# Kernel optimization log

Hardware: AMD Instinct MI355X
Metric: run time of the kernel (lower is better)

Reference implementation:

```python
import jax, jax.numpy as jnp
import numpy as np

NC, NG, NP = 8192, 4096, 140
FD, D, L = 512, 256, 2
E_OBS, E_COEXP, E_PPI, E_SYM = 300000, 200000, 10000, 20000
EPS = 1e-5


def layer_norm(x, g, b):
    mu = jnp.mean(x, -1, keepdims=True)
    v = jnp.mean((x - mu) ** 2, -1, keepdims=True)
    return (x - mu) * jax.lax.rsqrt(v + EPS) * g + b


def sage(h_src, h_dst, src, dst, w, Ws, Wn, b, n_dst):
    # DGL SAGEConv (mean aggregator, edge-weighted): mean over incoming
    # weighted messages, then fc_self(h_dst) + fc_neigh(neigh) + bias.
    m = h_src[src] * w[:, None]                                  # [E, D]
    neigh = jax.ops.segment_sum(m, dst, num_segments=n_dst)      # [n_dst, D]
    deg = jax.ops.segment_sum(jnp.ones_like(w), dst, num_segments=n_dst)
    neigh = neigh / jnp.maximum(deg, 1.0)[:, None]
    return h_dst @ Ws + neigh @ Wn + b


def setup_inputs() -> dict:
    key = jax.random.key(0)
    ks = iter(jax.random.split(key, 64))
    def n(*s):
        return jax.random.normal(next(ks), s, jnp.float32) * 0.02
    def u(e):
        return jax.random.uniform(next(ks), (e,), jnp.float32)
    def ri(e, hi):
        return jax.random.randint(next(ks), (e,), 0, hi, jnp.int32)
    return dict(
        cell_feat=jax.random.normal(next(ks), (NC, FD), jnp.float32),
        gene_feat=jax.random.normal(next(ks), (NG, FD), jnp.float32),
        pro_idx=jnp.arange(NP, dtype=jnp.int32),
        obs_src=ri(E_OBS, NG), obs_dst=ri(E_OBS, NC), obs_w=u(E_OBS),
        rev_obs_src=ri(E_OBS, NC), rev_obs_dst=ri(E_OBS, NG), rev_obs_w=u(E_OBS),
        symbol_src=ri(E_SYM, NG), symbol_dst=ri(E_SYM, NP), symbol_w=u(E_SYM),
        rev_symbol_src=ri(E_SYM, NP), rev_symbol_dst=ri(E_SYM, NG), rev_symbol_w=u(E_SYM),
        coexp_src=ri(E_COEXP, NG), coexp_dst=ri(E_COEXP, NG), coexp_w=u(E_COEXP),
        ppi_src=ri(E_PPI, NP), ppi_dst=ri(E_PPI, NP), ppi_w=u(E_PPI),
        W_emb_cell=n(FD, D), b_emb_cell=jnp.zeros((D,), jnp.float32),
        W_emb_gene=n(FD, D), b_emb_gene=jnp.zeros((D,), jnp.float32),
        emb_pro=n(NP, D),
        W_mlpcell=n(L, D, D), b_mlpcell=jnp.zeros((L, D), jnp.float32),
        W_sage_self=n(L, 6, D, D), W_sage_neigh=n(L, 6, D, D),
        b_sage=jnp.zeros((L, 6, D), jnp.float32),
        ln1_g=jnp.ones((L, 3, D), jnp.float32), ln1_b=jnp.zeros((L, 3, D), jnp.float32),
        ln2_g=jnp.ones((L, 3, D), jnp.float32), ln2_b=jnp.zeros((L, 3, D), jnp.float32),
        W_last=n(3 * D, NP), b_last=jnp.zeros((NP,), jnp.float32),
    )


def reference(cell_feat, gene_feat, pro_idx,
              obs_src, obs_dst, obs_w,
              rev_obs_src, rev_obs_dst, rev_obs_w,
              symbol_src, symbol_dst, symbol_w,
              rev_symbol_src, rev_symbol_dst, rev_symbol_w,
              coexp_src, coexp_dst, coexp_w,
              ppi_src, ppi_dst, ppi_w,
              W_emb_cell, b_emb_cell, W_emb_gene, b_emb_gene, emb_pro,
              W_mlpcell, b_mlpcell, W_sage_self, W_sage_neigh, b_sage,
              ln1_g, ln1_b, ln2_g, ln2_b, W_last, b_last):
    act = jax.nn.selu
    hc = cell_feat @ W_emb_cell + b_emb_cell      # emb_cell
    hg = gene_feat @ W_emb_gene + b_emb_gene      # emb_gene
    hp = emb_pro[pro_idx]                         # nn.Embedding path
    nc, ng, npn = hc.shape[0], hg.shape[0], hp.shape[0]
    hist = [hc]
    for l in range(W_mlpcell.shape[0]):
        Ws, Wn, bs = W_sage_self[l], W_sage_neigh[l], b_sage[l]
        hmlp = layer_norm(act(hc @ W_mlpcell[l] + b_mlpcell[l]), ln1_g[l, 2], ln1_b[l, 2])
        # HeteroGraphConv(SAGE) over edges_sub = [obs, rev_obs, symbol, rev_symbol] (stack)
        s_obs = sage(hg, hc, obs_src, obs_dst, obs_w, Ws[0], Wn[0], bs[0], nc)
        s_robs = sage(hc, hg, rev_obs_src, rev_obs_dst, rev_obs_w, Ws[1], Wn[1], bs[1], ng)
        s_sym = sage(hg, hp, symbol_src, symbol_dst, symbol_w, Ws[2], Wn[2], bs[2], npn)
        s_rsym = sage(hp, hg, rev_symbol_src, rev_symbol_dst, rev_symbol_w, Ws[3], Wn[3], bs[3], ng)
        # homogeneous subgraph convs: gene_sage on coexp, pro_sage on ppi
        h_gg = layer_norm(act(sage(hg, hg, coexp_src, coexp_dst, coexp_w, Ws[4], Wn[4], bs[4], ng)), ln1_g[l, 0], ln1_b[l, 0])
        h_pp = layer_norm(act(sage(hp, hp, ppi_src, ppi_dst, ppi_w, Ws[5], Wn[5], bs[5], npn)), ln1_g[l, 1], ln1_b[l, 1])
        # norm each stacked relation output, then agg='sum' over the stack dim
        hgen = layer_norm(act(s_robs), ln1_g[l, 0], ln1_b[l, 0]) + layer_norm(act(s_rsym), ln1_g[l, 0], ln1_b[l, 0]) + h_gg
        hpro = layer_norm(act(s_sym), ln1_g[l, 1], ln1_b[l, 1]) + h_pp
        hcel = layer_norm(act(s_obs), ln1_g[l, 2], ln1_b[l, 2]) + hmlp
        hg = layer_norm(act(hgen), ln2_g[l, 0], ln2_b[l, 0])
        hp = layer_norm(act(hpro), ln2_g[l, 1], ln2_b[l, 1])
        hc = layer_norm(act(hcel), ln2_g[l, 2], ln2_b[l, 2])
        hist.append(hc)
    # mlp_last over concat of per-layer cell reps (sum(dims[1:-1]) -> dims[-1])
    return jnp.concatenate(hist, -1) @ W_last + b_last
```

## Files before the change

kernel.cpp:

```cpp
#include <hip/hip_runtime.h>

typedef unsigned short ushort_t;
typedef unsigned int uint_t;

typedef ushort_t ushortx8 __attribute__((ext_vector_type(8)));
typedef ushort_t ushortx4 __attribute__((ext_vector_type(4)));
typedef __bf16 bf16x8 __attribute__((ext_vector_type(8)));
typedef float f32x4 __attribute__((ext_vector_type(4)));

#define NCC 8192
#define NGG 4096
#define NPP 140
#define LDS_STR 88

__device__ __forceinline__ float bf2f(ushort_t u) {
    uint_t i = ((uint_t)u) << 16;
    float f;
    __builtin_memcpy(&f, &i, 4);
    return f;
}
__device__ __forceinline__ ushort_t f2bf(float f) {
    uint_t i;
    __builtin_memcpy(&i, &f, 4);
    uint_t r = (i + 0x7FFFu + ((i >> 16) & 1u)) >> 16;
    return (ushort_t)r;
}
__device__ __forceinline__ float scrub(float x) {
    return __builtin_isfinite(x) ? x : 0.f;
}
__device__ __forceinline__ float selu_f(float x) {
    return x > 0.f ? 1.0507009873554805f * x : 1.7580993408473766f * expm1f(x);
}
__device__ __forceinline__ float wsum64(float x) {
    for (int o = 32; o; o >>= 1) x += __shfl_xor(x, o, 64);
    return x;
}

__global__ __launch_bounds__(256) void sc_zero1(int* __restrict__ a, int na) {
    int i = blockIdx.x * 256 + threadIdx.x;
    if (i < na) a[i] = 0;
}

struct CntJob {
    const int* dst;
    const int* src;
    const float* w;
    uint_t* pw;
    ushort_t* rank;
    int E;
    int* deg;
    int bstart;
};
struct CntBatch {
    CntJob j[6];
};
struct TrJob {
    const float* src;
    ushort_t* dst;
    int K, N, nx, nxy;
    int bstart;
};
struct TrBatch {
    TrJob j[6];
};
struct FillJob {
    const int* dst;
    const uint_t* pw;
    const ushort_t* rank;
    int E;
    const int* offs;
    uint_t* ep;
    int bstart;
};
struct FillBatch {
    FillJob j[6];
};
struct GemmJob {
    const void* A1;
    int lda1, K1, af1;
    const ushort_t* Bt1;
    const ushort_t* A2;
    int K2;
    const ushort_t* Bt2;
    const float* bias;
    ushort_t* C;
    int ldc, M;
    int mstart;
};
struct GemmBatch {
    GemmJob j[7];
};

struct PrepArgs {
    CntBatch cb;
    int bsC;
    TrBatch tb;
    int bsT;
    const float* emb;
    const int* pidx;
    ushort_t* hp;
    int nEmb;
};
__global__ __launch_bounds__(256) void sc_prep(PrepArgs pa) {
    __shared__ ushort_t t[32][33];
    int bx = blockIdx.x;
    if (bx < pa.bsC) {
        int r = 0;
#pragma unroll
        for (int i = 1; i < 6; ++i) r = (bx >= pa.cb.j[i].bstart) ? i : r;
        const CntJob& J = pa.cb.j[r];
        int e = (bx - J.bstart) * 256 + threadIdx.x;
        if (e < J.E) {
            int rk = atomicAdd(&J.deg[J.dst[e]], 1);
            J.rank[e] = (ushort_t)rk;
            J.pw[e] = ((uint_t)f2bf(J.w[e]) << 16) | (uint_t)J.src[e];
        }
        return;
    }
    bx -= pa.bsC;
    if (bx < pa.bsT) {
        int r = 0;
#pragma unroll
        for (int i = 1; i < 6; ++i) r = (bx >= pa.tb.j[i].bstart) ? i : r;
        const TrJob& J = pa.tb.j[r];
        int local = bx - J.bstart;
        int b = local / J.nxy, rem = local % J.nxy;
        int n0 = (rem % J.nx) * 32, k0 = (rem / J.nx) * 32;
        const float* s = J.src + (size_t)b * J.K * J.N;
        ushort_t* d = J.dst + (size_t)b * J.K * J.N;
        int x = threadIdx.x & 31, y = threadIdx.x >> 5;
        for (int i = y; i < 32; i += 8) {
            int k = k0 + i, n = n0 + x;
            t[i][x] = (k < J.K && n < J.N) ? f2bf(s[(size_t)k * J.N + n]) : (ushort_t)0;
        }
        __syncthreads();
        for (int i = y; i < 32; i += 8) {
            int n = n0 + i, k = k0 + x;
            if (n < J.N && k < J.K) d[(size_t)n * J.K + k] = t[x][i];
        }
        return;
    }
    bx -= pa.bsT;
    int i = bx * 256 + threadIdx.x;
    if (i < pa.nEmb) {
        int r = i >> 8, c = i & 255;
        int j = pa.pidx[r];
        j = (uint_t)j < (uint_t)NPP ? j : 0;
        pa.hp[i] = f2bf(pa.emb[(size_t)j * 256 + c]);
    }
}

__global__ __launch_bounds__(1024) void sc_csr_scan6(const int* __restrict__ deg_base,
                                                     int* __restrict__ offs_base) {
    const int ndst[6] = {NCC, NGG, NPP, NGG, NGG, NPP};
    const int dstart[6] = {0, NCC, NCC + NGG, NCC + NGG + NPP, NCC + 2 * NGG + NPP,
                           NCC + 3 * NGG + NPP};
    const int ostart[6] = {0, NCC + 1, NCC + NGG + 2, NCC + NGG + NPP + 3,
                           NCC + 2 * NGG + NPP + 4, NCC + 3 * NGG + NPP + 5};
    int r = blockIdx.x;
    const int* deg = deg_base + dstart[r];
    int* offs = offs_base + ostart[r];
    int n = ndst[r];
    __shared__ int wsum[16];
    __shared__ int carry;
    int tid = threadIdx.x, wave = tid >> 6, lane = tid & 63;
    if (tid == 0) carry = 0;
    __syncthreads();
    for (int base = 0; base < n; base += 1024) {
        int i = base + tid;
        int v = (i < n) ? deg[i] : 0;
        int x = v;
#pragma unroll
        for (int o = 1; o < 64; o <<= 1) {
            int tv = __shfl_up(x, o, 64);
            if (lane >= o) x += tv;
        }
        if (lane == 63) wsum[wave] = x;
        __syncthreads();
        if (tid == 0) {
            int acc = 0;
#pragma unroll
            for (int k = 0; k < 16; ++k) {
                int tv = wsum[k];
                wsum[k] = acc;
                acc += tv;
            }
        }
        __syncthreads();
        int incl = x + wsum[wave];
        int cr = carry;
        if (i < n) offs[i] = cr + incl - v;
        __syncthreads();
        if (tid == 1023) carry = cr + incl;
        __syncthreads();
    }
    if (tid == 0) offs[n] = carry;
}

__device__ __forceinline__ void gemm_body(const GemmBatch& gbat, int mbx, int n0, ushort_t* As,
                                          ushort_t* Bs) {
    int r = 0;
#pragma unroll
    for (int i = 1; i < 7; ++i) r = (mbx >= gbat.j[i].mstart) ? i : r;
    const void* JA1 = gbat.j[r].A1;
    const int lda1 = gbat.j[r].lda1, K1j = gbat.j[r].K1, af1 = gbat.j[r].af1;
    const ushort_t* JBt1 = gbat.j[r].Bt1;
    const ushort_t* JA2 = gbat.j[r].A2;
    const int K2j = gbat.j[r].K2;
    const ushort_t* JBt2 = gbat.j[r].Bt2;
    const float* bias = gbat.j[r].bias;
    ushort_t* C = gbat.j[r].C;
    const int ldc = gbat.j[r].ldc, M = gbat.j[r].M;
    const int tid = threadIdx.x;
    const int wave = tid >> 6, lane = tid & 63;
    const int lr = lane & 15, lq = lane >> 4;
    const int m0 = (mbx - gbat.j[r].mstart) * 128;
    f32x4 acc[2][4] = {};
    for (int pass = 0; pass < 2; ++pass) {
        const void* A = pass ? (const void*)JA2 : JA1;
        const ushort_t* Bt = pass ? JBt2 : JBt1;
        const int K = pass ? K2j : K1j;
        const int lda = pass ? 256 : lda1;
        const int af = pass ? 0 : af1;
        if (K == 0 || A == nullptr) continue;
        for (int k0 = 0; k0 < K; k0 += 64) {
            __syncthreads();
#pragma unroll
            for (int i = 0; i < 4; ++i) {
                int g = tid + i * 256;
                int rr = g >> 3, c = (g & 7) * 8;
                ushortx8 v = {0, 0, 0, 0, 0, 0, 0, 0};
                int gm = m0 + rr;
                if (gm < M) {
                    if (af) {
                        const float* Af = (const float*)A;
                        float4 f0 = *(const float4*)(Af + (size_t)gm * lda + k0 + c);
                        float4 f1 = *(const float4*)(Af + (size_t)gm * lda + k0 + c + 4);
                        v[0] = f2bf(f0.x);
                        v[1] = f2bf(f0.y);
                        v[2] = f2bf(f0.z);
                        v[3] = f2bf(f0.w);
                        v[4] = f2bf(f1.x);
                        v[5] = f2bf(f1.y);
                        v[6] = f2bf(f1.z);
                        v[7] = f2bf(f1.w);
                    } else {
                        v = *(const ushortx8*)((const ushort_t*)A + (size_t)gm * lda + k0 + c);
                    }
                }
                *(ushortx8*)(&As[rr * LDS_STR + c]) = v;
            }
#pragma unroll
            for (int i = 0; i < 2; ++i) {
                int g = tid + i * 256;
                int rr = g >> 3, c = (g & 7) * 8;
                int gn = n0 + rr;
                ushortx8 v = *(const ushortx8*)(Bt + (size_t)gn * K + k0 + c);
                *(ushortx8*)(&Bs[rr * LDS_STR + c]) = v;
            }
            __syncthreads();
#pragma unroll
            for (int kk = 0; kk < 64; kk += 32) {
                bf16x8 a0 = __builtin_bit_cast(
                    bf16x8, *(const ushortx8*)(&As[(wave * 32 + lr) * LDS_STR + kk + lq * 8]));
                bf16x8 a1 = __builtin_bit_cast(
                    bf16x8,
                    *(const ushortx8*)(&As[(wave * 32 + 16 + lr) * LDS_STR + kk + lq * 8]));
                bf16x8 b0 = __builtin_bit_cast(
                    bf16x8, *(const ushortx8*)(&Bs[(lr)*LDS_STR + kk + lq * 8]));
                bf16x8 b1 = __builtin_bit_cast(
                    bf16x8, *(const ushortx8*)(&Bs[(16 + lr) * LDS_STR + kk + lq * 8]));
                bf16x8 b2 = __builtin_bit_cast(
                    bf16x8, *(const ushortx8*)(&Bs[(32 + lr) * LDS_STR + kk + lq * 8]));
                bf16x8 b3 = __builtin_bit_cast(
                    bf16x8, *(const ushortx8*)(&Bs[(48 + lr) * LDS_STR + kk + lq * 8]));
                acc[0][0] = __builtin_amdgcn_mfma_f32_16x16x32_bf16(a0, b0, acc[0][0], 0, 0, 0);
                acc[0][1] = __builtin_amdgcn_mfma_f32_16x16x32_bf16(a0, b1, acc[0][1], 0, 0, 0);
                acc[0][2] = __builtin_amdgcn_mfma_f32_16x16x32_bf16(a0, b2, acc[0][2], 0, 0, 0);
                acc[0][3] = __builtin_amdgcn_mfma_f32_16x16x32_bf16(a0, b3, acc[0][3], 0, 0, 0);
                acc[1][0] = __builtin_amdgcn_mfma_f32_16x16x32_bf16(a1, b0, acc[1][0], 0, 0, 0);
                acc[1][1] = __builtin_amdgcn_mfma_f32_16x16x32_bf16(a1, b1, acc[1][1], 0, 0, 0);
                acc[1][2] = __builtin_amdgcn_mfma_f32_16x16x32_bf16(a1, b2, acc[1][2], 0, 0, 0);
                acc[1][3] = __builtin_amdgcn_mfma_f32_16x16x32_bf16(a1, b3, acc[1][3], 0, 0, 0);
            }
        }
    }
#pragma unroll
    for (int mt = 0; mt < 2; ++mt)
#pragma unroll
        for (int nt = 0; nt < 4; ++nt) {
            int col = n0 + nt * 16 + lr;
            float bb = bias[col];
#pragma unroll
            for (int v = 0; v < 4; ++v) {
                int row = m0 + wave * 32 + mt * 16 + lq * 4 + v;
                if (row >= M) continue;
                C[(size_t)row * ldc + col] = f2bf(scrub(acc[mt][nt][v] + bb));
            }
        }
}

__global__ __launch_bounds__(256) void sc_gemm_batch(GemmBatch gbat) {
    __shared__ __align__(16) ushort_t As[128 * LDS_STR];
    __shared__ __align__(16) ushort_t Bs[64 * LDS_STR];
    gemm_body(gbat, blockIdx.x, blockIdx.y * 64, As, Bs);
}

struct FillGemmArgs {
    GemmBatch gb;
    int gemmBlocks;
    FillBatch fb;
};
__global__ __launch_bounds__(256) void sc_fill_gemm(FillGemmArgs fg) {
    __shared__ __align__(16) ushort_t As[128 * LDS_STR];
    __shared__ __align__(16) ushort_t Bs[64 * LDS_STR];
    int bx = blockIdx.x;
    if (bx >= fg.gemmBlocks) {
        bx -= fg.gemmBlocks;
        int r = 0;
#pragma unroll
        for (int i = 1; i < 6; ++i) r = (bx >= fg.fb.j[i].bstart) ? i : r;
        const FillJob& J = fg.fb.j[r];
        int e = (bx - J.bstart) * 256 + threadIdx.x;
        if (e < J.E) {
            int d = J.dst[e];
            J.ep[J.offs[d] + (int)J.rank[e]] = J.pw[e];
        }
        return;
    }
    gemm_body(fg.gb, bx >> 2, (bx & 3) * 64, As, Bs);
}

struct GatherJob {
    const ushort_t* hsrc;
    int src_ld, src_n;
    const int* offs;
    const uint_t* ep;
    ushort_t* out;
    int row_start;
};
struct GatherBatch {
    GatherJob j[6];
};
__global__ __launch_bounds__(256) void sc_gather_all(GatherBatch gb, int total_rows) {
    int grow = blockIdx.x * 4 + (threadIdx.x >> 6);
    if (grow >= total_rows) return;
    int r = 0;
#pragma unroll
    for (int i = 1; i < 6; ++i) r = (grow >= gb.j[i].row_start) ? i : r;
    r = __builtin_amdgcn_readfirstlane(r);
    const ushort_t* hsrc = gb.j[r].hsrc;
    const int src_ld = gb.j[r].src_ld, src_n = gb.j[r].src_n;
    const int* offs = gb.j[r].offs;
    const uint_t* ep = gb.j[r].ep;
    ushort_t* out = gb.j[r].out;
    int row = grow - gb.j[r].row_start;
    int lane = threadIdx.x & 63, c = lane * 4;
    int s0 = offs[row], s1 = offs[row + 1];
    float a0 = 0.f, a1 = 0.f, a2 = 0.f, a3 = 0.f;
    for (int base = s0; base < s1; base += 64) {
        int e = base + lane;
        uint_t myp = (e < s1) ? ep[e] : 0u;
        int cnt = s1 - base;
        cnt = cnt < 64 ? cnt : 64;
        int cnt16 = (cnt + 15) & ~15;
        for (int jj = 0; jj < cnt16; jj += 16) {
#pragma unroll
            for (int u = 0; u < 16; ++u) {
                uint_t pw = (uint_t)__shfl((int)myp, jj + u, 64);
                int s = (int)(pw & 0xFFFFu);
                s = (uint_t)s < (uint_t)src_n ? s : 0;
                float w = bf2f((ushort_t)(pw >> 16));
                ushortx4 v = *(const ushortx4*)(hsrc + (size_t)s * src_ld + c);
                a0 += w * bf2f(v[0]);
                a1 += w * bf2f(v[1]);
                a2 += w * bf2f(v[2]);
                a3 += w * bf2f(v[3]);
            }
        }
    }
    float inv = 1.f / fmaxf((float)(s1 - s0), 1.f);
    ushort_t* o = out + (size_t)row * 256 + c;
    o[0] = f2bf(scrub(a0 * inv));
    o[1] = f2bf(scrub(a1 * inv));
    o[2] = f2bf(scrub(a2 * inv));
    o[3] = f2bf(scrub(a3 * inv));
}

__global__ __launch_bounds__(256) void sc_gemm(const ushort_t* __restrict__ A1, int lda1,
                                               const ushort_t* __restrict__ Bt1, int K1,
                                               const float* __restrict__ bias,
                                               float* __restrict__ Cf, int ldc, int M, int N) {
    __shared__ __align__(16) ushort_t As[128 * LDS_STR];
    __shared__ __align__(16) ushort_t Bs[64 * LDS_STR];
    const int tid = threadIdx.x;
    const int wave = tid >> 6, lane = tid & 63;
    const int lr = lane & 15, lq = lane >> 4;
    const int m0 = blockIdx.x * 128, n0 = blockIdx.y * 64;
    f32x4 acc[2][4] = {};
    for (int k0 = 0; k0 < K1; k0 += 64) {
        __syncthreads();
#pragma unroll
        for (int i = 0; i < 4; ++i) {
            int g = tid + i * 256;
            int r = g >> 3, c = (g & 7) * 8;
            ushortx8 v = {0, 0, 0, 0, 0, 0, 0, 0};
            int gm = m0 + r;
            if (gm < M) v = *(const ushortx8*)(A1 + (size_t)gm * lda1 + k0 + c);
            *(ushortx8*)(&As[r * LDS_STR + c]) = v;
        }
#pragma unroll
        for (int i = 0; i < 2; ++i) {
            int g = tid + i * 256;
            int r = g >> 3, c = (g & 7) * 8;
            ushortx8 v = {0, 0, 0, 0, 0, 0, 0, 0};
            int gn = n0 + r;
            if (gn < N) v = *(const ushortx8*)(Bt1 + (size_t)gn * K1 + k0 + c);
            *(ushortx8*)(&Bs[r * LDS_STR + c]) = v;
        }
        __syncthreads();
#pragma unroll
        for (int kk = 0; kk < 64; kk += 32) {
            bf16x8 a0 = __builtin_bit_cast(
                bf16x8, *(const ushortx8*)(&As[(wave * 32 + lr) * LDS_STR + kk + lq * 8]));
            bf16x8 a1 = __builtin_bit_cast(
                bf16x8, *(const ushortx8*)(&As[(wave * 32 + 16 + lr) * LDS_STR + kk + lq * 8]));
            bf16x8 b0 =
                __builtin_bit_cast(bf16x8, *(const ushortx8*)(&Bs[(lr)*LDS_STR + kk + lq * 8]));
            bf16x8 b1 = __builtin_bit_cast(
                bf16x8, *(const ushortx8*)(&Bs[(16 + lr) * LDS_STR + kk + lq * 8]));
            bf16x8 b2 = __builtin_bit_cast(
                bf16x8, *(const ushortx8*)(&Bs[(32 + lr) * LDS_STR + kk + lq * 8]));
            bf16x8 b3 = __builtin_bit_cast(
                bf16x8, *(const ushortx8*)(&Bs[(48 + lr) * LDS_STR + kk + lq * 8]));
            acc[0][0] = __builtin_amdgcn_mfma_f32_16x16x32_bf16(a0, b0, acc[0][0], 0, 0, 0);
            acc[0][1] = __builtin_amdgcn_mfma_f32_16x16x32_bf16(a0, b1, acc[0][1], 0, 0, 0);
            acc[0][2] = __builtin_amdgcn_mfma_f32_16x16x32_bf16(a0, b2, acc[0][2], 0, 0, 0);
            acc[0][3] = __builtin_amdgcn_mfma_f32_16x16x32_bf16(a0, b3, acc[0][3], 0, 0, 0);
            acc[1][0] = __builtin_amdgcn_mfma_f32_16x16x32_bf16(a1, b0, acc[1][0], 0, 0, 0);
            acc[1][1] = __builtin_amdgcn_mfma_f32_16x16x32_bf16(a1, b1, acc[1][1], 0, 0, 0);
            acc[1][2] = __builtin_amdgcn_mfma_f32_16x16x32_bf16(a1, b2, acc[1][2], 0, 0, 0);
            acc[1][3] = __builtin_amdgcn_mfma_f32_16x16x32_bf16(a1, b3, acc[1][3], 0, 0, 0);
        }
    }
#pragma unroll
    for (int mt = 0; mt < 2; ++mt)
#pragma unroll
        for (int nt = 0; nt < 4; ++nt) {
            int col = n0 + nt * 16 + lr;
            if (col >= N) continue;
            float bb = bias ? bias[col] : 0.f;
#pragma unroll
            for (int v = 0; v < 4; ++v) {
                int row = m0 + wave * 32 + mt * 16 + lq * 4 + v;
                if (row >= M) continue;
                Cf[(size_t)row * ldc + col] = scrub(acc[mt][nt][v] + bb);
            }
        }
}

struct LnJob {
    const ushort_t *sA, *sB, *sC;
    const float *g1, *b1, *g2, *b2;
    ushort_t* out;
    int out_ld;
    int row_start;
};
struct LnBatch {
    LnJob j[3];
};
__global__ __launch_bounds__(256) void sc_fuse_ln_all(LnBatch lb, int total_rows) {
    int grow = blockIdx.x * 4 + (threadIdx.x >> 6);
    if (grow >= total_rows) return;
    int r = 0;
#pragma unroll
    for (int i = 1; i < 3; ++i) r = (grow >= lb.j[i].row_start) ? i : r;
    r = __builtin_amdgcn_readfirstlane(r);
    const ushort_t* srcs[3] = {lb.j[r].sA, lb.j[r].sB, lb.j[r].sC};
    const float* g1 = lb.j[r].g1;
    const float* b1 = lb.j[r].b1;
    const float* g2 = lb.j[r].g2;
    const float* b2 = lb.j[r].b2;
    ushort_t* out = lb.j[r].out;
    int out_ld = lb.j[r].out_ld;
    int row = grow - lb.j[r].row_start;
    int lane = threadIdx.x & 63, c = lane * 4;
    float t[4] = {0.f, 0.f, 0.f, 0.f};
#pragma unroll
    for (int si = 0; si < 3; ++si) {
        const ushort_t* s = srcs[si];
        if (!s) continue;
        ushortx4 v = *(const ushortx4*)(s + (size_t)row * 256 + c);
        float x0 = selu_f(scrub(bf2f(v[0]))), x1 = selu_f(scrub(bf2f(v[1])));
        float x2 = selu_f(scrub(bf2f(v[2]))), x3 = selu_f(scrub(bf2f(v[3])));
        float mu = wsum64(x0 + x1 + x2 + x3) * (1.f / 256.f);
        float d0 = x0 - mu, d1 = x1 - mu, d2 = x2 - mu, d3 = x3 - mu;
        float var = wsum64(d0 * d0 + d1 * d1 + d2 * d2 + d3 * d3) * (1.f / 256.f);
        float rr = rsqrtf(var + 1e-5f);
        t[0] += d0 * rr * g1[c + 0] + b1[c + 0];
        t[1] += d1 * rr * g1[c + 1] + b1[c + 1];
        t[2] += d2 * rr * g1[c + 2] + b1[c + 2];
        t[3] += d3 * rr * g1[c + 3] + b1[c + 3];
    }
    float x0 = selu_f(scrub(t[0])), x1 = selu_f(scrub(t[1]));
    float x2 = selu_f(scrub(t[2])), x3 = selu_f(scrub(t[3]));
    float mu = wsum64(x0 + x1 + x2 + x3) * (1.f / 256.f);
    float d0 = x0 - mu, d1 = x1 - mu, d2 = x2 - mu, d3 = x3 - mu;
    float var = wsum64(d0 * d0 + d1 * d1 + d2 * d2 + d3 * d3) * (1.f / 256.f);
    float rr = rsqrtf(var + 1e-5f);
    ushort_t* o = out + (size_t)row * out_ld + c;
    o[0] = f2bf(scrub(d0 * rr * g2[c + 0] + b2[c + 0]));
    o[1] = f2bf(scrub(d1 * rr * g2[c + 1] + b2[c + 1]));
    o[2] = f2bf(scrub(d2 * rr * g2[c + 2] + b2[c + 2]));
    o[3] = f2bf(scrub(d3 * rr * g2[c + 3] + b2[c + 3]));
}

static inline int cdivi(int a, int b) { return (a + b - 1) / b; }

extern "C" void kernel_launch(void* const* d_in, const int* in_sizes, int n_in, void* d_out,
                              int out_size, void* d_ws, size_t ws_size, hipStream_t stream) {
    const float* cell_feat = (const float*)d_in[0];
    const float* gene_feat = (const float*)d_in[1];
    const int* pro_idx = (const int*)d_in[2];
    const int* edge_src[6] = {(const int*)d_in[3],  (const int*)d_in[6],  (const int*)d_in[9],
                              (const int*)d_in[12], (const int*)d_in[15], (const int*)d_in[18]};
    const int* edge_dst[6] = {(const int*)d_in[4],  (const int*)d_in[7],  (const int*)d_in[10],
                              (const int*)d_in[13], (const int*)d_in[16], (const int*)d_in[19]};
    const float* edge_w[6] = {(const float*)d_in[5],  (const float*)d_in[8],
                              (const float*)d_in[11], (const float*)d_in[14],
                              (const float*)d_in[17], (const float*)d_in[20]};
    const float* W_emb_cell = (const float*)d_in[21];
    const float* b_emb_cell = (const float*)d_in[22];
    const float* W_emb_gene = (const float*)d_in[23];
    const float* b_emb_gene = (const float*)d_in[24];
    const float* emb_pro = (const float*)d_in[25];
    const float* W_mlpcell = (const float*)d_in[26];
    const float* b_mlpcell = (const float*)d_in[27];
    const float* W_sage_self = (const float*)d_in[28];
    const float* W_sage_neigh = (const float*)d_in[29];
    const float* b_sage = (const float*)d_in[30];
    const float* ln1_g = (const float*)d_in[31];
    const float* ln1_b = (const float*)d_in[32];
    const float* ln2_g = (const float*)d_in[33];
    const float* ln2_b = (const float*)d_in[34];
    const float* W_last = (const float*)d_in[35];
    const float* b_last = (const float*)d_in[36];

    const int E_obs = in_sizes[3], E_sym = in_sizes[9], E_coexp = in_sizes[15],
              E_ppi = in_sizes[18];
    const int Er[6] = {E_obs, E_obs, E_sym, E_sym, E_coexp, E_ppi};
    const int Nd[6] = {NCC, NGG, NPP, NGG, NGG, NPP};

    char* p = (char*)d_ws;
    auto carve = [&](size_t bytes) -> char* {
        char* r = p;
        p += ((bytes + 255) & ~(size_t)255);
        return r;
    };
    ushort_t* hist = (ushort_t*)carve((size_t)NCC * 768 * 2);
    ushort_t* hg = (ushort_t*)carve((size_t)NGG * 256 * 2);
    ushort_t* hp = (ushort_t*)carve((size_t)NPP * 256 * 2);
    ushort_t* n_obs = (ushort_t*)carve((size_t)NCC * 256 * 2);
    ushort_t* n_robs = (ushort_t*)carve((size_t)NGG * 256 * 2);
    ushort_t* n_sym = (ushort_t*)carve((size_t)NPP * 256 * 2);
    ushort_t* n_rsym = (ushort_t*)carve((size_t)NGG * 256 * 2);
    ushort_t* n_coexp = (ushort_t*)carve((size_t)NGG * 256 * 2);
    ushort_t* n_ppi = (ushort_t*)carve((size_t)NPP * 256 * 2);
    ushort_t* s_obs = (ushort_t*)carve((size_t)NCC * 256 * 2);
    ushort_t* s_robs = (ushort_t*)carve((size_t)NGG * 256 * 2);
    ushort_t* s_sym = (ushort_t*)carve((size_t)NPP * 256 * 2);
    ushort_t* s_rsym = (ushort_t*)carve((size_t)NGG * 256 * 2);
    ushort_t* s_coexp = (ushort_t*)carve((size_t)NGG * 256 * 2);
    ushort_t* s_ppi = (ushort_t*)carve((size_t)NPP * 256 * 2);
    ushort_t* s_mlp = (ushort_t*)carve((size_t)NCC * 256 * 2);
    ushort_t* Wt_emb_cell = (ushort_t*)carve((size_t)512 * 256 * 2);
    ushort_t* Wt_emb_gene = (ushort_t*)carve((size_t)512 * 256 * 2);
    ushort_t* Wt_mlp = (ushort_t*)carve((size_t)2 * 256 * 256 * 2);
    ushort_t* Wt_self = (ushort_t*)carve((size_t)12 * 256 * 256 * 2);
    ushort_t* Wt_neigh = (ushort_t*)carve((size_t)12 * 256 * 256 * 2);
    ushort_t* Wt_last = (ushort_t*)carve((size_t)140 * 768 * 2);
    const int NDTOT = NCC + 3 * NGG + 2 * NPP;
    int* deg_all = (int*)carve((size_t)NDTOT * 4);
    int* offs_all = (int*)carve((size_t)(NDTOT + 6) * 4);
    const int ETOT = 2 * E_obs + 2 * E_sym + E_coexp + E_ppi;
    uint_t* pw_all = (uint_t*)carve((size_t)ETOT * 4);
    ushort_t* rank_all = (ushort_t*)carve((size_t)ETOT * 2);
    uint_t* ep_all = (uint_t*)carve((size_t)ETOT * 4);
    (void)ws_size;
    (void)n_in;
    (void)out_size;

    const int dS[6] = {0, NCC, NCC + NGG, NCC + NGG + NPP, NCC + 2 * NGG + NPP,
                       NCC + 3 * NGG + NPP};
    const int oS[6] = {0, NCC + 1, NCC + NGG + 2, NCC + NGG + NPP + 3, NCC + 2 * NGG + NPP + 4,
                       NCC + 3 * NGG + NPP + 5};
    int eS[6];
    eS[0] = 0;
    eS[1] = eS[0] + E_obs;
    eS[2] = eS[1] + E_obs;
    eS[3] = eS[2] + E_sym;
    eS[4] = eS[3] + E_sym;
    eS[5] = eS[4] + E_coexp;

    sc_zero1<<<cdivi(NDTOT, 256), 256, 0, stream>>>(deg_all, NDTOT);
    {
        PrepArgs pa;
        int bs = 0;
        for (int r = 0; r < 6; ++r) {
            pa.cb.j[r] = {edge_dst[r], edge_src[r], edge_w[r], pw_all + eS[r], rank_all + eS[r],
                          Er[r], deg_all + dS[r], bs};
            bs += cdivi(Er[r], 256);
        }
        pa.bsC = bs;
        int bt = 0;
        auto add = [&](int idx, const float* s, ushort_t* d, int B, int K, int N) {
            int nx = cdivi(N, 32), ny = cdivi(K, 32);
            pa.tb.j[idx] = {s, d, K, N, nx, nx * ny, bt};
            bt += B * nx * ny;
        };
        add(0, W_emb_cell, Wt_emb_cell, 1, 512, 256);
        add(1, W_emb_gene, Wt_emb_gene, 1, 512, 256);
        add(2, W_mlpcell, Wt_mlp, 2, 256, 256);
        add(3, W_sage_self, Wt_self, 12, 256, 256);
        add(4, W_sage_neigh, Wt_neigh, 12, 256, 256);
        add(5, W_last, Wt_last, 1, 768, 140);
        pa.bsT = bt;
        pa.emb = emb_pro;
        pa.pidx = pro_idx;
        pa.hp = hp;
        pa.nEmb = NPP * 256;
        int bsE = cdivi(NPP * 256, 256);
        sc_prep<<<pa.bsC + pa.bsT + bsE, 256, 0, stream>>>(pa);
    }
    sc_csr_scan6<<<6, 1024, 0, stream>>>(deg_all, offs_all);
    {
        FillGemmArgs fg;
        for (int i = 0; i < 7; ++i) fg.gb.j[i].mstart = 0x7FFFFFFF;
        fg.gb.j[0] = {cell_feat, 512, 512, 1, Wt_emb_cell, nullptr, 0, nullptr, b_emb_cell, hist,
                      768, NCC, 0};
        fg.gb.j[1] = {gene_feat, 512, 512, 1, Wt_emb_gene, nullptr, 0, nullptr, b_emb_gene, hg,
                      256, NGG, 64};
        fg.gemmBlocks = 96 * 4;
        int bs = 0;
        for (int r = 0; r < 6; ++r) {
            fg.fb.j[r] = {edge_dst[r], pw_all + eS[r], rank_all + eS[r], Er[r], offs_all + oS[r],
                          ep_all + eS[r], bs};
            bs += cdivi(Er[r], 256);
        }
        sc_fill_gemm<<<fg.gemmBlocks + bs, 256, 0, stream>>>(fg);
    }

    for (int l = 0; l < 2; ++l) {
        const ushort_t* hc_l = hist + l * 256;
        {
            GatherBatch gb;
            const ushort_t* hs[6] = {hg, hc_l, hg, hp, hg, hp};
            const int lds[6] = {256, 768, 256, 256, 256, 256};
            const int sn[6] = {NGG, NCC, NGG, NPP, NGG, NPP};
            ushort_t* outs[6] = {n_obs, n_robs, n_sym, n_rsym, n_coexp, n_ppi};
            int rs = 0;
            for (int r = 0; r < 6; ++r) {
                gb.j[r] = {hs[r], lds[r], sn[r], offs_all + oS[r], ep_all + eS[r], outs[r], rs};
                rs += Nd[r];
            }
            sc_gather_all<<<cdivi(rs, 4), 256, 0, stream>>>(gb, rs);
        }
        {
            const size_t WSZ = 65536;
            GemmBatch gbat;
            gbat.j[0] = {hc_l, 768, 256, 0, Wt_mlp + (size_t)l * WSZ, nullptr, 0, nullptr,
                         b_mlpcell + l * 256, s_mlp, 256, NCC, 0};
            const ushort_t* dstf[6] = {hc_l, hg, hp, hg, hg, hp};
            const int dld[6] = {768, 256, 256, 256, 256, 256};
            const ushort_t* nb[6] = {n_obs, n_robs, n_sym, n_rsym, n_coexp, n_ppi};
            ushort_t* so[6] = {s_obs, s_robs, s_sym, s_rsym, s_coexp, s_ppi};
            int ms = cdivi(NCC, 128);
            for (int r = 0; r < 6; ++r) {
                gbat.j[r + 1] = {dstf[r],
                                 dld[r],
                                 256,
                                 0,
                                 Wt_self + (size_t)(l * 6 + r) * WSZ,
                                 nb[r],
                                 256,
                                 Wt_neigh + (size_t)(l * 6 + r) * WSZ,
                                 b_sage + (l * 6 + r) * 256,
                                 so[r],
                                 256,
                                 Nd[r],
                                 ms};
                ms += cdivi(Nd[r], 128);
            }
            sc_gemm_batch<<<dim3(ms, 4), 256, 0, stream>>>(gbat);
        }
        {
            LnBatch lb;
            lb.j[0] = {s_robs, s_rsym, s_coexp, ln1_g + (l * 3 + 0) * 256,
                       ln1_b + (l * 3 + 0) * 256, ln2_g + (l * 3 + 0) * 256,
                       ln2_b + (l * 3 + 0) * 256, hg, 256, 0};
            lb.j[1] = {s_sym, s_ppi, nullptr, ln1_g + (l * 3 + 1) * 256,
                       ln1_b + (l * 3 + 1) * 256, ln2_g + (l * 3 + 1) * 256,
                       ln2_b + (l * 3 + 1) * 256, hp, 256, NGG};
            lb.j[2] = {s_obs, s_mlp, nullptr, ln1_g + (l * 3 + 2) * 256,
                       ln1_b + (l * 3 + 2) * 256, ln2_g + (l * 3 + 2) * 256,
                       ln2_b + (l * 3 + 2) * 256, hist + (l + 1) * 256, 768, NGG + NPP};
            int rs = NGG + NPP + NCC;
            sc_fuse_ln_all<<<cdivi(rs, 4), 256, 0, stream>>>(lb, rs);
        }
    }

    sc_gemm<<<dim3(64, 3), 256, 0, stream>>>(hist, 768, Wt_last, 768, b_last, (float*)d_out, 140,
                                             NCC, 140);
}
```

Measured before the change: 422.1 us.

## Count edge degrees with per-block LDS histograms before global atomics

Moves degree counting and edge-rank assignment out of the prep kernel into a new kernel. Each 1024-thread block histograms 16K edges in shared memory, then issues one global atomic per nonzero bin to reserve a base offset, and ranks become base plus local rank. This is meant to cut global atomic contention on the degree array. It adds a kernel launch and uses 32KB of LDS per block, and the count work no longer overlaps with the transpose work.

After: 391.9 us. -7.2%, faster.

```diff
diff --git a/kernel.cpp b/kernel.cpp
--- a/kernel.cpp
+++ b/kernel.cpp
@@ -12,6 +12,7 @@
 #define NGG 4096
 #define NPP 140
 #define LDS_STR 88
+#define CEPB 16384
 
 __device__ __forceinline__ float bf2f(ushort_t u) {
     uint_t i = ((uint_t)u) << 16;
@@ -41,18 +42,19 @@
     if (i < na) a[i] = 0;
 }
 
-struct CntJob {
+struct CountJob {
     const int* dst;
     const int* src;
     const float* w;
     uint_t* pw;
     ushort_t* rank;
     int E;
+    int nbins;
     int* deg;
     int bstart;
 };
-struct CntBatch {
-    CntJob j[6];
+struct CountBatch {
+    CountJob j[6];
 };
 struct TrJob {
     const float* src;
@@ -91,9 +93,45 @@
     GemmJob j[7];
 };
 
+__global__ __launch_bounds__(1024) void sc_count(CountBatch cb) {
+    __shared__ int hist[NCC];
+    int bx = blockIdx.x;
+    int r = 0;
+#pragma unroll
+    for (int i = 1; i < 6; ++i) r = (bx >= cb.j[i].bstart) ? i : r;
+    const CountJob& J = cb.j[r];
+    const int nb = J.nbins;
+    const int tid = threadIdx.x;
+    for (int b = tid; b < nb; b += 1024) hist[b] = 0;
+    __syncthreads();
+    const int e0 = (bx - J.bstart) * CEPB;
+    ushort_t lr[16];
+#pragma unroll
+    for (int u = 0; u < 16; ++u) {
+        int e = e0 + u * 1024 + tid;
+        if (e < J.E) {
+            int d = J.dst[e];
+            lr[u] = (ushort_t)atomicAdd(&hist[d], 1);
+            J.pw[e] = ((uint_t)f2bf(J.w[e]) << 16) | (uint_t)J.src[e];
+        }
+    }
+    __syncthreads();
+    for (int b = tid; b < nb; b += 1024) {
+        int c = hist[b];
+        if (c > 0) hist[b] = atomicAdd(&J.deg[b], c);
+    }
+    __syncthreads();
+#pragma unroll
+    for (int u = 0; u < 16; ++u) {
+        int e = e0 + u * 1024 + tid;
+        if (e < J.E) {
+            int d = J.dst[e];
+            J.rank[e] = (ushort_t)(hist[d] + (int)lr[u]);
+        }
+    }
+}
+
 struct PrepArgs {
-    CntBatch cb;
-    int bsC;
     TrBatch tb;
     int bsT;
     const float* emb;
@@ -104,20 +142,6 @@
 __global__ __launch_bounds__(256) void sc_prep(PrepArgs pa) {
     __shared__ ushort_t t[32][33];
     int bx = blockIdx.x;
-    if (bx < pa.bsC) {
-        int r = 0;
-#pragma unroll
-        for (int i = 1; i < 6; ++i) r = (bx >= pa.cb.j[i].bstart) ? i : r;
-        const CntJob& J = pa.cb.j[r];
-        int e = (bx - J.bstart) * 256 + threadIdx.x;
-        if (e < J.E) {
-            int rk = atomicAdd(&J.deg[J.dst[e]], 1);
-            J.rank[e] = (ushort_t)rk;
-            J.pw[e] = ((uint_t)f2bf(J.w[e]) << 16) | (uint_t)J.src[e];
-        }
-        return;
-    }
-    bx -= pa.bsC;
     if (bx < pa.bsT) {
         int r = 0;
 #pragma unroll
@@ -604,14 +628,17 @@
 
     sc_zero1<<<cdivi(NDTOT, 256), 256, 0, stream>>>(deg_all, NDTOT);
     {
-        PrepArgs pa;
+        CountBatch cb;
         int bs = 0;
         for (int r = 0; r < 6; ++r) {
-            pa.cb.j[r] = {edge_dst[r], edge_src[r], edge_w[r], pw_all + eS[r], rank_all + eS[r],
-                          Er[r], deg_all + dS[r], bs};
-            bs += cdivi(Er[r], 256);
-        }
-        pa.bsC = bs;
+            cb.j[r] = {edge_dst[r], edge_src[r], edge_w[r], pw_all + eS[r], rank_all + eS[r],
+                       Er[r],       Nd[r],       deg_all + dS[r], bs};
+            bs += cdivi(Er[r], CEPB);
+        }
+        sc_count<<<bs, 1024, 0, stream>>>(cb);
+    }
+    {
+        PrepArgs pa;
         int bt = 0;
         auto add = [&](int idx, const float* s, ushort_t* d, int B, int K, int N) {
             int nx = cdivi(N, 32), ny = cdivi(K, 32);
@@ -630,7 +657,7 @@
         pa.hp = hp;
         pa.nEmb = NPP * 256;
         int bsE = cdivi(NPP * 256, 256);
-        sc_prep<<<pa.bsC + pa.bsT + bsE, 256, 0, stream>>>(pa);
+        sc_prep<<<pa.bsT + bsE, 256, 0, stream>>>(pa);
     }
     sc_csr_scan6<<<6, 1024, 0, stream>>>(deg_all, offs_all);
     {
```
